# Kernel optimization log

Measured on AMD Instinct MI355X. Metric: run time of the kernel, lower is better.

Reference implementation:

```python
import jax, jax.numpy as jnp
import numpy as np

CUTOFF = 3.5          # angular_cutoff (init kwarg)
EPS = 1e-7            # keras.backend.epsilon()
CLIP_MIN = 1e-10      # tf.clip_by_value min on Carnot denominators
B, N = 8, 32
MLP_DIMS = [(9, 64), (64, 64), (64, 64), (64, 64), (64, 64), (64, 128), (128, 256)]


def _he(key, fan_in, fan_out):
    return jax.random.normal(key, (fan_in, fan_out), jnp.float32) * np.float32(np.sqrt(2.0 / fan_in))


def setup_inputs() -> dict:
    key = jax.random.key(0)
    k_pos, k_sp, k_w, k_b = jax.random.split(key, 4)
    # realistic symmetric distance matrix with zero diagonal, from random 3D positions
    pos = jax.random.uniform(k_pos, (B, N, 3), jnp.float32) * 9.0
    diff = pos[:, :, None, :] - pos[:, None, :, :]
    D = jnp.sqrt(jnp.sum(diff * diff, axis=-1) + 1e-12)
    D = D * (1.0 - jnp.eye(N, dtype=jnp.float32))
    species = jax.random.randint(k_sp, (B, N), 1, 10).astype(jnp.float32)
    inp = {"distance_matrices": D, "num_species_batch": species}
    for i, (fi, fo) in enumerate(MLP_DIMS):
        inp[f"W{i}"] = _he(jax.random.fold_in(k_w, i), fi, fo)
        inp[f"b{i}"] = jax.random.normal(jax.random.fold_in(k_b, i), (fo,), jnp.float32) * 0.01
    return inp


def _ang_mlp(x, W0, b0, W1, b1, W2, b2, W3, b3, W4, b4, W5, b5, W6, b6):
    # residual MLP: 9 -> 64 (x5, two residual adds) -> 128 -> 256, all tanh
    x_res = jnp.tanh(x @ W0 + b0)
    x1 = jnp.tanh(x_res @ W1 + b1)
    xb1 = x1 + x_res
    x2 = jnp.tanh(xb1 @ W2 + b2)
    x3 = jnp.tanh(x2 @ W3 + b3)
    x4 = jnp.tanh(x3 @ W4 + b4)
    xb2 = x4 + xb1
    xb3 = jnp.tanh(xb2 @ W5 + b5)
    return jnp.tanh(xb3 @ W6 + b6)


def _forward(D, S, W0, b0, W1, b1, W2, b2, W3, b3, W4, b4, W5, b5, W6, b6):
    n = D.shape[-1]
    ji, ki = jnp.triu_indices(n, k=1)                       # P = n(n-1)/2 ordered pairs j<k
    cm = (D < CUTOFF) & (D != 0.0)                          # [B,N,N]
    mask = cm[:, :, ji] & cm[:, :, ki]                      # [B,N,P] valid triplets (i;j,k)
    R_ij = D[:, :, ji]                                      # [B,N,P]
    R_ik = D[:, :, ki]
    R_jk = jnp.broadcast_to(D[:, ji, ki][:, None, :], R_ij.shape)
    z_i = jnp.broadcast_to(S[:, :, None], R_ij.shape)
    z_j = jnp.broadcast_to(S[:, ji][:, None, :], R_ij.shape)
    z_k = jnp.broadcast_to(S[:, ki][:, None, :], R_ij.shape)
    # Carnot formula for the three cosines of the triangle (i,j,k)
    clip = lambda d: jnp.maximum(d, CLIP_MIN)
    c_i = (R_ij**2 + R_ik**2 - R_jk**2) / clip(2.0 * R_ij * R_ik)
    c_j = (R_ij**2 + R_jk**2 - R_ik**2) / clip(2.0 * R_ij * R_jk)
    c_k = (R_ik**2 + R_jk**2 - R_ij**2) / clip(2.0 * R_ik * R_jk)
    geo = jnp.stack([
        R_ij + R_ik + R_jk,
        R_ij * R_ik + R_ij * R_jk + R_ik * R_jk,
        R_ij * R_ik * R_jk,
    ], axis=-1)                                             # [B,N,P,3]
    chem = jnp.stack([
        z_i + z_j + z_k,
        c_i + c_j + c_k,
        z_i * (z_j + z_k) + z_j * z_k - c_i * (c_j + c_k) - c_j * c_k,
        z_i * (c_j + c_k) + c_i * (z_j + z_k) + z_j * c_k + c_j * z_k,
        z_i * (z_j * z_k - c_j * c_k) - c_i * (z_j * c_k + c_j * z_k),
        z_i * (z_j * c_k + c_j * z_k) + c_i * (z_j * z_k - c_j * c_k),
    ], axis=-1)                                             # [B,N,P,6]
    geo = geo / (jnp.linalg.norm(geo, axis=-1, keepdims=True) + EPS)
    chem = chem / (jnp.linalg.norm(chem, axis=-1, keepdims=True) + EPS)
    feat = jnp.concatenate([geo, chem], axis=-1)            # [B,N,P,9]
    out = _ang_mlp(feat, W0, b0, W1, b1, W2, b2, W3, b3, W4, b4, W5, b5, W6, b6)  # [B,N,P,256]
    f_c = lambda d: 0.5 * jnp.cos(np.float32(np.pi) * d / CUTOFF) + 0.5
    w = jnp.where(mask, f_c(R_ij) * f_c(R_ik), 0.0)[..., None]
    GA = jnp.sum(out * w, axis=2)                           # scatter-add over triplets -> [B,N,256]
    return GA / (jnp.linalg.norm(GA, axis=-1, keepdims=True) + EPS)


def reference(distance_matrices, num_species_batch, W0, b0, W1, b1, W2, b2, W3, b3, W4, b4, W5, b5, W6, b6):
    return _forward(distance_matrices, num_species_batch, W0, b0, W1, b1, W2, b2, W3, b3, W4, b4, W5, b5, W6, b6)
```

## Files before the change

### kernel.cpp

```cpp
#include <hip/hip_runtime.h>
#include <math.h>

#define NB 8
#define NA 32
#define NCELL 256
#define NPAIR 496
#define SLOT 496
#define FST 10
#define TC 16
#define XS 20
#define NQ 8
#define CUTOFF_F 3.5f
#define EPS_F 1e-7f
#define CLIP_MIN_F 1e-10f
#define PI_F 3.14159274101257324f

__global__ __launch_bounds__(256) void aev_feat(
    const float* __restrict__ D, const float* __restrict__ S,
    float* __restrict__ feat, int* __restrict__ count, float* __restrict__ GA)
{
    __shared__ float Dm[NA][NA];
    __shared__ float Sv[NA];
    __shared__ int s_T;
    const int tid = threadIdx.x;
    const int cell = blockIdx.x;
    const int b = cell >> 5, i = cell & 31;

    for (int idx = tid; idx < NA * NA; idx += 256)
        ((float*)Dm)[idx] = D[b * NA * NA + idx];
    if (tid < NA) Sv[tid] = S[b * NA + tid];
    if (tid == 0) s_T = 0;
    GA[cell * 256 + tid] = 0.f;
    __syncthreads();

    for (int p = tid; p < NPAIR; p += 256) {
        int rem = p, j = 0;
        while (rem >= 31 - j) { rem -= 31 - j; ++j; }
        const int k = j + 1 + rem;
        const float dij = Dm[i][j], dik = Dm[i][k];
        if (dij < CUTOFF_F && dij != 0.f && dik < CUTOFF_F && dik != 0.f) {
            const int slot = atomicAdd(&s_T, 1);
            const float Rij = dij, Rik = dik, Rjk = Dm[j][k];
            const float zi = Sv[i], zj = Sv[j], zk = Sv[k];
            const float ci = (Rij*Rij + Rik*Rik - Rjk*Rjk) / fmaxf(2.f*Rij*Rik, CLIP_MIN_F);
            const float cj = (Rij*Rij + Rjk*Rjk - Rik*Rik) / fmaxf(2.f*Rij*Rjk, CLIP_MIN_F);
            const float ck = (Rik*Rik + Rjk*Rjk - Rij*Rij) / fmaxf(2.f*Rik*Rjk, CLIP_MIN_F);
            float g0 = Rij + Rik + Rjk;
            float g1 = Rij*Rik + Rij*Rjk + Rik*Rjk;
            float g2 = Rij*Rik*Rjk;
            const float gn = sqrtf(g0*g0 + g1*g1 + g2*g2) + EPS_F;
            float h0 = zi + zj + zk;
            float h1 = ci + cj + ck;
            float h2 = zi*(zj + zk) + zj*zk - ci*(cj + ck) - cj*ck;
            float h3 = zi*(cj + ck) + ci*(zj + zk) + zj*ck + cj*zk;
            float h4 = zi*(zj*zk - cj*ck) - ci*(zj*ck + cj*zk);
            float h5 = zi*(zj*ck + cj*zk) + ci*(zj*zk - cj*ck);
            const float hn = sqrtf(h0*h0 + h1*h1 + h2*h2 + h3*h3 + h4*h4 + h5*h5) + EPS_F;
            const float fcij = 0.5f * cosf(PI_F * Rij / CUTOFF_F) + 0.5f;
            const float fcik = 0.5f * cosf(PI_F * Rik / CUTOFF_F) + 0.5f;
            float* fp = &feat[(cell * SLOT + slot) * FST];
            fp[0] = g0 / gn; fp[1] = g1 / gn; fp[2] = g2 / gn;
            fp[3] = h0 / hn; fp[4] = h1 / hn; fp[5] = h2 / hn;
            fp[6] = h3 / hn; fp[7] = h4 / hn; fp[8] = h5 / hn;
            fp[9] = fcij * fcik;
        }
    }
    __syncthreads();
    if (tid == 0) count[cell] = s_T;
}

__device__ __forceinline__ void cp_async16(const float* g, float* l) {
    __builtin_amdgcn_global_load_lds(
        (const __attribute__((address_space(1))) unsigned int*)g,
        (__attribute__((address_space(3))) unsigned int*)l, 16, 0, 0);
}

__device__ __forceinline__ void stage16k(const float* __restrict__ g,
                                         float* __restrict__ buf, int tid) {
    const int lane = tid & 63, w = tid >> 6;
#pragma unroll
    for (int r = 0; r < 4; ++r) {
        const int off = (w * 4 + r) * 256;
        cp_async16(g + off + lane * 4, buf + off);
    }
}

template<int K, bool RES>
__device__ __forceinline__ void compute64(
    const float* __restrict__ Wl, const float* __restrict__ bl,
    const float* __restrict__ X, float* __restrict__ Y,
    const float* __restrict__ R, int tid)
{
    const int fi = tid & 63;
    const int xo = (tid >> 6) * 4;
    const float bb = bl[fi];
    float a0 = bb, a1 = bb, a2 = bb, a3 = bb;
#pragma unroll 4
    for (int k = 0; k < K; ++k) {
        const float4 xv = *(const float4*)&X[k * XS + xo];
        const float w = Wl[k * 64 + fi];
        a0 += xv.x * w; a1 += xv.y * w; a2 += xv.z * w; a3 += xv.w * w;
    }
    float4 y;
    y.x = tanhf(a0); y.y = tanhf(a1); y.z = tanhf(a2); y.w = tanhf(a3);
    if (RES) {
        const float4 r = *(const float4*)&R[fi * XS + xo];
        y.x += r.x; y.y += r.y; y.z += r.z; y.w += r.w;
    }
    *(float4*)&Y[fi * XS + xo] = y;
}

__device__ __forceinline__ void compute5_part(
    const float* __restrict__ Wl , const float* __restrict__ X,
    int k0, float (&a0)[4], float (&a1)[4], int tid)
{
    const int fo = tid & 63;
    const int xo = (tid >> 6) * 4;
#pragma unroll 4
    for (int k = 0; k < 32; ++k) {
        const float4 xv = *(const float4*)&X[(k0 + k) * XS + xo];
        const float w0 = Wl[k * 128 + fo];
        const float w1 = Wl[k * 128 + fo + 64];
        a0[0] += xv.x * w0; a0[1] += xv.y * w0; a0[2] += xv.z * w0; a0[3] += xv.w * w0;
        a1[0] += xv.x * w1; a1[1] += xv.y * w1; a1[2] += xv.z * w1; a1[3] += xv.w * w1;
    }
}

__device__ __forceinline__ void compute6_part(
    const float* __restrict__ Wl , const float* __restrict__ X,
    int k0, float (&a)[16], int tid)
{
#pragma unroll 2
    for (int k = 0; k < 16; ++k) {
        const float w = Wl[k * 256 + tid];
        const float4 x0 = *(const float4*)&X[(k0 + k) * XS + 0];
        const float4 x1 = *(const float4*)&X[(k0 + k) * XS + 4];
        const float4 x2 = *(const float4*)&X[(k0 + k) * XS + 8];
        const float4 x3 = *(const float4*)&X[(k0 + k) * XS + 12];
        a[0]  += x0.x * w; a[1]  += x0.y * w; a[2]  += x0.z * w; a[3]  += x0.w * w;
        a[4]  += x1.x * w; a[5]  += x1.y * w; a[6]  += x1.z * w; a[7]  += x1.w * w;
        a[8]  += x2.x * w; a[9]  += x2.y * w; a[10] += x2.z * w; a[11] += x2.w * w;
        a[12] += x3.x * w; a[13] += x3.y * w; a[14] += x3.z * w; a[15] += x3.w * w;
    }
}

__global__ __launch_bounds__(256, 2) void aev_mlp(
    const float* __restrict__ feat, const int* __restrict__ count,
    const float* __restrict__ W0, const float* __restrict__ b0,
    const float* __restrict__ W1, const float* __restrict__ b1,
    const float* __restrict__ W2, const float* __restrict__ b2,
    const float* __restrict__ W3, const float* __restrict__ b3,
    const float* __restrict__ W4, const float* __restrict__ b4,
    const float* __restrict__ W5, const float* __restrict__ b5,
    const float* __restrict__ W6, const float* __restrict__ b6,
    float* __restrict__ GA)
{
    __shared__ __align__(16) float WB0[4096];
    __shared__ __align__(16) float WB1[4096];
    __shared__ __align__(16) float WB2[4096];
    __shared__ __align__(16) float Xs[9 * XS];
    __shared__ __align__(16) float U0[64 * XS];
    __shared__ __align__(16) float U1[64 * XS];
    __shared__ __align__(16) float U2[64 * XS];
    __shared__ __align__(16) float U3[128 * XS];
    __shared__ float wsh[TC];
    __shared__ float bsh[704];

    const int tid = threadIdx.x;
    const int cell = blockIdx.x & 255;
    const int q = blockIdx.x >> 8;
    const int T = count[cell];
    const int nch = (T + TC - 1) / TC;
    if (q >= nch) return;

    if (tid < 64) {
        bsh[tid]       = b0[tid];
        bsh[64 + tid]  = b1[tid];
        bsh[128 + tid] = b2[tid];
        bsh[192 + tid] = b3[tid];
        bsh[256 + tid] = b4[tid];
    }
    if (tid < 128) bsh[320 + tid] = b5[tid];
    bsh[448 + tid] = b6[tid];

    float gacc = 0.f;

    for (int c = q; c < nch; c += NQ) {
        const int t0 = c * TC;

        stage16k(W1, WB1, tid);
        if (tid < 144) ((float4*)WB0)[tid] = ((const float4*)W0)[tid];
        if (tid < TC * FST) {
            const int t = tid / FST, qf = tid % FST;
            const int slot = t0 + t;
            const float v = (slot < T) ? feat[(cell * SLOT + t0) * FST + tid] : 0.f;
            if (qf == 9) wsh[t] = v; else Xs[qf * XS + t] = v;
        }
        __syncthreads();

        stage16k(W2, WB2, tid);
        compute64<9,  false>(WB0, bsh + 0,   Xs, U0, nullptr, tid);
        __syncthreads();
        stage16k(W3, WB0, tid);
        compute64<64, true >(WB1, bsh + 64,  U0, U1, U0, tid);
        __syncthreads();
        stage16k(W4, WB1, tid);
        compute64<64, false>(WB2, bsh + 128, U1, U2, nullptr, tid);
        __syncthreads();
        stage16k(W5, WB2, tid);
        compute64<64, false>(WB0, bsh + 192, U2, U0, nullptr, tid);
        __syncthreads();
        stage16k(W5 + 4096, WB0, tid);
        compute64<64, true >(WB1, bsh + 256, U0, U2, U1, tid);
        __syncthreads();

        float a0[4], a1[4];
        {
            const int fo = tid & 63;
            const float bb0 = bsh[320 + fo], bb1 = bsh[320 + fo + 64];
#pragma unroll
            for (int r = 0; r < 4; ++r) { a0[r] = bb0; a1[r] = bb1; }
        }
        stage16k(W6, WB1, tid);
        compute5_part(WB2, U2, 0, a0, a1, tid);
        __syncthreads();
        stage16k(W6 + 4096, WB2, tid);
        compute5_part(WB0, U2, 32, a0, a1, tid);
        {
            const int fo = tid & 63;
            const int xo = (tid >> 6) * 4;
            float4 y0, y1;
            y0.x = tanhf(a0[0]); y0.y = tanhf(a0[1]); y0.z = tanhf(a0[2]); y0.w = tanhf(a0[3]);
            y1.x = tanhf(a1[0]); y1.y = tanhf(a1[1]); y1.z = tanhf(a1[2]); y1.w = tanhf(a1[3]);
            *(float4*)&U3[fo * XS + xo] = y0;
            *(float4*)&U3[(fo + 64) * XS + xo] = y1;
        }
        __syncthreads();

        float a6[16];
        {
            const float bb = bsh[448 + tid];
#pragma unroll
            for (int r = 0; r < 16; ++r) a6[r] = bb;
        }
        stage16k(W6 + 2 * 4096, WB0, tid);
        compute6_part(WB1, U3, 0, a6, tid);
        __syncthreads();
        stage16k(W6 + 3 * 4096, WB1, tid);
        compute6_part(WB2, U3, 16, a6, tid);
        __syncthreads();
        stage16k(W6 + 4 * 4096, WB2, tid);
        compute6_part(WB0, U3, 32, a6, tid);
        __syncthreads();
        stage16k(W6 + 5 * 4096, WB0, tid);
        compute6_part(WB1, U3, 48, a6, tid);
        __syncthreads();
        stage16k(W6 + 6 * 4096, WB1, tid);
        compute6_part(WB2, U3, 64, a6, tid);
        __syncthreads();
        stage16k(W6 + 7 * 4096, WB2, tid);
        compute6_part(WB0, U3, 80, a6, tid);
        __syncthreads();
        compute6_part(WB1, U3, 96, a6, tid);
        __syncthreads();
        compute6_part(WB2, U3, 112, a6, tid);

#pragma unroll 4
        for (int r = 0; r < 16; ++r)
            gacc += wsh[r] * tanhf(a6[r]);
        __syncthreads();
    }

    atomicAdd(&GA[cell * 256 + tid], gacc);
}

__global__ __launch_bounds__(256) void aev_norm(
    const float* __restrict__ GA, float* __restrict__ out)
{
    __shared__ float wred[4];
    const int tid = threadIdx.x;
    const int cell = blockIdx.x;
    const float v = GA[cell * 256 + tid];
    float ss = v * v;
#pragma unroll
    for (int off = 32; off > 0; off >>= 1) ss += __shfl_down(ss, off);
    if ((tid & 63) == 0) wred[tid >> 6] = ss;
    __syncthreads();
    const float tot = wred[0] + wred[1] + wred[2] + wred[3];
    out[cell * 256 + tid] = v / (sqrtf(tot) + EPS_F);
}

extern "C" void kernel_launch(void* const* d_in, const int* in_sizes, int n_in,
                              void* d_out, int out_size, void* d_ws, size_t ws_size,
                              hipStream_t stream)
{
    const float* D  = (const float*)d_in[0];
    const float* S  = (const float*)d_in[1];
    const float* W0 = (const float*)d_in[2];  const float* b0 = (const float*)d_in[3];
    const float* W1 = (const float*)d_in[4];  const float* b1 = (const float*)d_in[5];
    const float* W2 = (const float*)d_in[6];  const float* b2 = (const float*)d_in[7];
    const float* W3 = (const float*)d_in[8];  const float* b3 = (const float*)d_in[9];
    const float* W4 = (const float*)d_in[10]; const float* b4 = (const float*)d_in[11];
    const float* W5 = (const float*)d_in[12]; const float* b5 = (const float*)d_in[13];
    const float* W6 = (const float*)d_in[14]; const float* b6 = (const float*)d_in[15];
    float* out = (float*)d_out;

    float* feat  = (float*)d_ws;
    int*   count = (int*)(feat + NCELL * SLOT * FST);
    float* GA    = (float*)(count + 256);

    aev_feat<<<dim3(NCELL), dim3(256), 0, stream>>>(D, S, feat, count, GA);
    aev_mlp<<<dim3(NCELL * NQ), dim3(256), 0, stream>>>(
        feat, count, W0, b0, W1, b1, W2, b2, W3, b3, W4, b4, W5, b5, W6, b6, GA);
    aev_norm<<<dim3(NCELL), dim3(256), 0, stream>>>(GA, out);
}
```

Baseline: 117.9 us.

## Double triplet chunk size and retile MLP layers for larger per-thread register tiles

Raises the per-chunk triplet tile from 16 to 32, so each staged weight block in shared memory is reused across twice as many triplets. Per-thread register tiles grow to 8 columns in the 64-wide layers and to 2×16 outputs in the 256-wide layer. The grid is reorganised to four blocks per cell instead of eight, and the launch bound asking for two blocks per SM is dropped. This cuts weight staging and synchronisation per triplet, but raises register pressure and lowers block count and occupancy.

```diff
diff --git a/kernel.cpp b/kernel.cpp
--- a/kernel.cpp
+++ b/kernel.cpp
@@ -7,9 +7,9 @@
 #define NPAIR 496
 #define SLOT 496
 #define FST 10
-#define TC 16
-#define XS 20
-#define NQ 8
+#define TC 32
+#define XS 36
+#define NQ 4
 #define CUTOFF_F 3.5f
 #define EPS_F 1e-7f
 #define CLIP_MIN_F 1e-10f
@@ -92,59 +92,74 @@
     const float* __restrict__ R, int tid)
 {
     const int fi = tid & 63;
-    const int xo = (tid >> 6) * 4;
+    const int xo = (tid >> 6) * 8;
     const float bb = bl[fi];
-    float a0 = bb, a1 = bb, a2 = bb, a3 = bb;
+    float a[8];
+#pragma unroll
+    for (int r = 0; r < 8; ++r) a[r] = bb;
 #pragma unroll 4
     for (int k = 0; k < K; ++k) {
-        const float4 xv = *(const float4*)&X[k * XS + xo];
+        const float4 x0 = *(const float4*)&X[k * XS + xo];
+        const float4 x1 = *(const float4*)&X[k * XS + xo + 4];
         const float w = Wl[k * 64 + fi];
-        a0 += xv.x * w; a1 += xv.y * w; a2 += xv.z * w; a3 += xv.w * w;
-    }
-    float4 y;
-    y.x = tanhf(a0); y.y = tanhf(a1); y.z = tanhf(a2); y.w = tanhf(a3);
+        a[0] += x0.x * w; a[1] += x0.y * w; a[2] += x0.z * w; a[3] += x0.w * w;
+        a[4] += x1.x * w; a[5] += x1.y * w; a[6] += x1.z * w; a[7] += x1.w * w;
+    }
+    float4 y0, y1;
+    y0.x = tanhf(a[0]); y0.y = tanhf(a[1]); y0.z = tanhf(a[2]); y0.w = tanhf(a[3]);
+    y1.x = tanhf(a[4]); y1.y = tanhf(a[5]); y1.z = tanhf(a[6]); y1.w = tanhf(a[7]);
     if (RES) {
-        const float4 r = *(const float4*)&R[fi * XS + xo];
-        y.x += r.x; y.y += r.y; y.z += r.z; y.w += r.w;
-    }
-    *(float4*)&Y[fi * XS + xo] = y;
+        const float4 r0 = *(const float4*)&R[fi * XS + xo];
+        const float4 r1 = *(const float4*)&R[fi * XS + xo + 4];
+        y0.x += r0.x; y0.y += r0.y; y0.z += r0.z; y0.w += r0.w;
+        y1.x += r1.x; y1.y += r1.y; y1.z += r1.z; y1.w += r1.w;
+    }
+    *(float4*)&Y[fi * XS + xo]     = y0;
+    *(float4*)&Y[fi * XS + xo + 4] = y1;
 }
 
 __device__ __forceinline__ void compute5_part(
     const float* __restrict__ Wl , const float* __restrict__ X,
-    int k0, float (&a0)[4], float (&a1)[4], int tid)
+    int k0, float (&a0)[8], float (&a1)[8], int tid)
 {
     const int fo = tid & 63;
-    const int xo = (tid >> 6) * 4;
-#pragma unroll 4
+    const int xo = (tid >> 6) * 8;
+#pragma unroll 2
     for (int k = 0; k < 32; ++k) {
-        const float4 xv = *(const float4*)&X[(k0 + k) * XS + xo];
+        const float4 x0 = *(const float4*)&X[(k0 + k) * XS + xo];
+        const float4 x1 = *(const float4*)&X[(k0 + k) * XS + xo + 4];
         const float w0 = Wl[k * 128 + fo];
         const float w1 = Wl[k * 128 + fo + 64];
-        a0[0] += xv.x * w0; a0[1] += xv.y * w0; a0[2] += xv.z * w0; a0[3] += xv.w * w0;
-        a1[0] += xv.x * w1; a1[1] += xv.y * w1; a1[2] += xv.z * w1; a1[3] += xv.w * w1;
+        a0[0] += x0.x * w0; a0[1] += x0.y * w0; a0[2] += x0.z * w0; a0[3] += x0.w * w0;
+        a0[4] += x1.x * w0; a0[5] += x1.y * w0; a0[6] += x1.z * w0; a0[7] += x1.w * w0;
+        a1[0] += x0.x * w1; a1[1] += x0.y * w1; a1[2] += x0.z * w1; a1[3] += x0.w * w1;
+        a1[4] += x1.x * w1; a1[5] += x1.y * w1; a1[6] += x1.z * w1; a1[7] += x1.w * w1;
     }
 }
 
 __device__ __forceinline__ void compute6_part(
     const float* __restrict__ Wl , const float* __restrict__ X,
-    int k0, float (&a)[16], int tid)
+    int fo, int to, float (&a0)[16], float (&a1)[16])
 {
 #pragma unroll 2
     for (int k = 0; k < 16; ++k) {
-        const float w = Wl[k * 256 + tid];
-        const float4 x0 = *(const float4*)&X[(k0 + k) * XS + 0];
-        const float4 x1 = *(const float4*)&X[(k0 + k) * XS + 4];
-        const float4 x2 = *(const float4*)&X[(k0 + k) * XS + 8];
-        const float4 x3 = *(const float4*)&X[(k0 + k) * XS + 12];
-        a[0]  += x0.x * w; a[1]  += x0.y * w; a[2]  += x0.z * w; a[3]  += x0.w * w;
-        a[4]  += x1.x * w; a[5]  += x1.y * w; a[6]  += x1.z * w; a[7]  += x1.w * w;
-        a[8]  += x2.x * w; a[9]  += x2.y * w; a[10] += x2.z * w; a[11] += x2.w * w;
-        a[12] += x3.x * w; a[13] += x3.y * w; a[14] += x3.z * w; a[15] += x3.w * w;
-    }
-}
-
-__global__ __launch_bounds__(256, 2) void aev_mlp(
+        const float2 wv = *(const float2*)&Wl[k * 256 + fo];
+        const float4 x0 = *(const float4*)&X[k * XS + to];
+        const float4 x1 = *(const float4*)&X[k * XS + to + 4];
+        const float4 x2 = *(const float4*)&X[k * XS + to + 8];
+        const float4 x3 = *(const float4*)&X[k * XS + to + 12];
+        a0[0]  += x0.x * wv.x; a0[1]  += x0.y * wv.x; a0[2]  += x0.z * wv.x; a0[3]  += x0.w * wv.x;
+        a0[4]  += x1.x * wv.x; a0[5]  += x1.y * wv.x; a0[6]  += x1.z * wv.x; a0[7]  += x1.w * wv.x;
+        a0[8]  += x2.x * wv.x; a0[9]  += x2.y * wv.x; a0[10] += x2.z * wv.x; a0[11] += x2.w * wv.x;
+        a0[12] += x3.x * wv.x; a0[13] += x3.y * wv.x; a0[14] += x3.z * wv.x; a0[15] += x3.w * wv.x;
+        a1[0]  += x0.x * wv.y; a1[1]  += x0.y * wv.y; a1[2]  += x0.z * wv.y; a1[3]  += x0.w * wv.y;
+        a1[4]  += x1.x * wv.y; a1[5]  += x1.y * wv.y; a1[6]  += x1.z * wv.y; a1[7]  += x1.w * wv.y;
+        a1[8]  += x2.x * wv.y; a1[9]  += x2.y * wv.y; a1[10] += x2.z * wv.y; a1[11] += x2.w * wv.y;
+        a1[12] += x3.x * wv.y; a1[13] += x3.y * wv.y; a1[14] += x3.z * wv.y; a1[15] += x3.w * wv.y;
+    }
+}
+
+__global__ __launch_bounds__(256) void aev_mlp(
     const float* __restrict__ feat, const int* __restrict__ count,
     const float* __restrict__ W0, const float* __restrict__ b0,
     const float* __restrict__ W1, const float* __restrict__ b1,
@@ -167,8 +182,8 @@
     __shared__ float bsh[704];
 
     const int tid = threadIdx.x;
-    const int cell = blockIdx.x & 255;
-    const int q = blockIdx.x >> 8;
+    const int cell = blockIdx.x >> 2;
+    const int q = blockIdx.x & 3;
     const int T = count[cell];
     const int nch = (T + TC - 1) / TC;
     if (q >= nch) return;
@@ -183,17 +198,19 @@
     if (tid < 128) bsh[320 + tid] = b5[tid];
     bsh[448 + tid] = b6[tid];
 
-    float gacc = 0.f;
+    const int fo6 = (tid & 127) * 2;
+    const int to6 = (tid >> 7) * 16;
+    float gacc0 = 0.f, gacc1 = 0.f;
 
     for (int c = q; c < nch; c += NQ) {
         const int t0 = c * TC;
 
         stage16k(W1, WB1, tid);
         if (tid < 144) ((float4*)WB0)[tid] = ((const float4*)W0)[tid];
-        if (tid < TC * FST) {
-            const int t = tid / FST, qf = tid % FST;
+        for (int idx = tid; idx < TC * FST; idx += 256) {
+            const int t = idx / FST, qf = idx % FST;
             const int slot = t0 + t;
-            const float v = (slot < T) ? feat[(cell * SLOT + t0) * FST + tid] : 0.f;
+            const float v = (slot < T) ? feat[(cell * SLOT + t0) * FST + idx] : 0.f;
             if (qf == 9) wsh[t] = v; else Xs[qf * XS + t] = v;
         }
         __syncthreads();
@@ -214,12 +231,12 @@
         compute64<64, true >(WB1, bsh + 256, U0, U2, U1, tid);
         __syncthreads();
 
-        float a0[4], a1[4];
+        float a0[8], a1[8];
         {
             const int fo = tid & 63;
             const float bb0 = bsh[320 + fo], bb1 = bsh[320 + fo + 64];
 #pragma unroll
-            for (int r = 0; r < 4; ++r) { a0[r] = bb0; a1[r] = bb1; }
+            for (int r = 0; r < 8; ++r) { a0[r] = bb0; a1[r] = bb1; }
         }
         stage16k(W6, WB1, tid);
         compute5_part(WB2, U2, 0, a0, a1, tid);
@@ -228,50 +245,60 @@
         compute5_part(WB0, U2, 32, a0, a1, tid);
         {
             const int fo = tid & 63;
-            const int xo = (tid >> 6) * 4;
+            const int xo = (tid >> 6) * 8;
             float4 y0, y1;
             y0.x = tanhf(a0[0]); y0.y = tanhf(a0[1]); y0.z = tanhf(a0[2]); y0.w = tanhf(a0[3]);
-            y1.x = tanhf(a1[0]); y1.y = tanhf(a1[1]); y1.z = tanhf(a1[2]); y1.w = tanhf(a1[3]);
-            *(float4*)&U3[fo * XS + xo] = y0;
-            *(float4*)&U3[(fo + 64) * XS + xo] = y1;
-        }
-        __syncthreads();
-
-        float a6[16];
+            y1.x = tanhf(a0[4]); y1.y = tanhf(a0[5]); y1.z = tanhf(a0[6]); y1.w = tanhf(a0[7]);
+            *(float4*)&U3[fo * XS + xo]     = y0;
+            *(float4*)&U3[fo * XS + xo + 4] = y1;
+            y0.x = tanhf(a1[0]); y0.y = tanhf(a1[1]); y0.z = tanhf(a1[2]); y0.w = tanhf(a1[3]);
+            y1.x = tanhf(a1[4]); y1.y = tanhf(a1[5]); y1.z = tanhf(a1[6]); y1.w = tanhf(a1[7]);
+            *(float4*)&U3[(fo + 64) * XS + xo]     = y0;
+            *(float4*)&U3[(fo + 64) * XS + xo + 4] = y1;
+        }
+        __syncthreads();
+
+        float c0[16], c1[16];
         {
-            const float bb = bsh[448 + tid];
-#pragma unroll
-            for (int r = 0; r < 16; ++r) a6[r] = bb;
+            const float bb0 = bsh[448 + fo6], bb1 = bsh[448 + fo6 + 1];
+#pragma unroll
+            for (int r = 0; r < 16; ++r) { c0[r] = bb0; c1[r] = bb1; }
         }
         stage16k(W6 + 2 * 4096, WB0, tid);
-        compute6_part(WB1, U3, 0, a6, tid);
+        compute6_part(WB1, U3 + 0 * XS * 16 + 0, fo6, to6, c0, c1);
         __syncthreads();
         stage16k(W6 + 3 * 4096, WB1, tid);
-        compute6_part(WB2, U3, 16, a6, tid);
+        compute6_part(WB2, U3 + 16 * XS, fo6, to6, c0, c1);
         __syncthreads();
         stage16k(W6 + 4 * 4096, WB2, tid);
-        compute6_part(WB0, U3, 32, a6, tid);
+        compute6_part(WB0, U3 + 32 * XS, fo6, to6, c0, c1);
         __syncthreads();
         stage16k(W6 + 5 * 4096, WB0, tid);
-        compute6_part(WB1, U3, 48, a6, tid);
+        compute6_part(WB1, U3 + 48 * XS, fo6, to6, c0, c1);
         __syncthreads();
         stage16k(W6 + 6 * 4096, WB1, tid);
-        compute6_part(WB2, U3, 64, a6, tid);
+        compute6_part(WB2, U3 + 64 * XS, fo6, to6, c0, c1);
         __syncthreads();
         stage16k(W6 + 7 * 4096, WB2, tid);
-        compute6_part(WB0, U3, 80, a6, tid);
-        __syncthreads();
-        compute6_part(WB1, U3, 96, a6, tid);
-        __syncthreads();
-        compute6_part(WB2, U3, 112, a6, tid);
-
+        compute6_part(WB0, U3 + 80 * XS, fo6, to6, c0, c1);
+        __syncthreads();
+        compute6_part(WB1, U3 + 96 * XS, fo6, to6, c0, c1);
+        __syncthreads();
+        compute6_part(WB2, U3 + 112 * XS, fo6, to6, c0, c1);
+
+        float s0 = 0.f, s1 = 0.f;
 #pragma unroll 4
-        for (int r = 0; r < 16; ++r)
-            gacc += wsh[r] * tanhf(a6[r]);
-        __syncthreads();
-    }
-
-    atomicAdd(&GA[cell * 256 + tid], gacc);
+        for (int r = 0; r < 16; ++r) {
+            const float wt = wsh[to6 + r];
+            s0 += wt * tanhf(c0[r]);
+            s1 += wt * tanhf(c1[r]);
+        }
+        gacc0 += s0; gacc1 += s1;
+        __syncthreads();
+    }
+
+    atomicAdd(&GA[cell * 256 + fo6], gacc0);
+    atomicAdd(&GA[cell * 256 + fo6 + 1], gacc1);
 }
 
 __global__ __launch_bounds__(256) void aev_norm(
```

New measurement: 223.8 us. 89.9% more time.

## Shrink MLP shared memory to double-buffered weights and register biases

Applied to the files above, without the earlier changes.

Replaces the triple-buffered weight staging with two 16 KB buffers plus a small persistent W0 copy, and reuses U0/U1 in place of the separate U3 buffer. Biases now live in registers instead of a shared array. The launch-bounds minimum-blocks hint is dropped. The intent is to cut LDS use so more blocks fit per CU, at the cost of a shallower prefetch pipeline (one stage ahead instead of two) and extra register pressure.

```diff
diff --git a/kernel.cpp b/kernel.cpp
--- a/kernel.cpp
+++ b/kernel.cpp
@@ -87,13 +87,12 @@
 
 template<int K, bool RES>
 __device__ __forceinline__ void compute64(
-    const float* __restrict__ Wl, const float* __restrict__ bl,
+    const float* __restrict__ Wl, float bb,
     const float* __restrict__ X, float* __restrict__ Y,
     const float* __restrict__ R, int tid)
 {
     const int fi = tid & 63;
     const int xo = (tid >> 6) * 4;
-    const float bb = bl[fi];
     float a0 = bb, a1 = bb, a2 = bb, a3 = bb;
 #pragma unroll 4
     for (int k = 0; k < K; ++k) {
@@ -128,15 +127,15 @@
 
 __device__ __forceinline__ void compute6_part(
     const float* __restrict__ Wl , const float* __restrict__ X,
-    int k0, float (&a)[16], int tid)
+    float (&a)[16], int tid)
 {
 #pragma unroll 2
     for (int k = 0; k < 16; ++k) {
         const float w = Wl[k * 256 + tid];
-        const float4 x0 = *(const float4*)&X[(k0 + k) * XS + 0];
-        const float4 x1 = *(const float4*)&X[(k0 + k) * XS + 4];
-        const float4 x2 = *(const float4*)&X[(k0 + k) * XS + 8];
-        const float4 x3 = *(const float4*)&X[(k0 + k) * XS + 12];
+        const float4 x0 = *(const float4*)&X[k * XS + 0];
+        const float4 x1 = *(const float4*)&X[k * XS + 4];
+        const float4 x2 = *(const float4*)&X[k * XS + 8];
+        const float4 x3 = *(const float4*)&X[k * XS + 12];
         a[0]  += x0.x * w; a[1]  += x0.y * w; a[2]  += x0.z * w; a[3]  += x0.w * w;
         a[4]  += x1.x * w; a[5]  += x1.y * w; a[6]  += x1.z * w; a[7]  += x1.w * w;
         a[8]  += x2.x * w; a[9]  += x2.y * w; a[10] += x2.z * w; a[11] += x2.w * w;
@@ -144,7 +143,7 @@
     }
 }
 
-__global__ __launch_bounds__(256, 2) void aev_mlp(
+__global__ __launch_bounds__(256) void aev_mlp(
     const float* __restrict__ feat, const int* __restrict__ count,
     const float* __restrict__ W0, const float* __restrict__ b0,
     const float* __restrict__ W1, const float* __restrict__ b1,
@@ -155,16 +154,14 @@
     const float* __restrict__ W6, const float* __restrict__ b6,
     float* __restrict__ GA)
 {
-    __shared__ __align__(16) float WB0[4096];
-    __shared__ __align__(16) float WB1[4096];
-    __shared__ __align__(16) float WB2[4096];
+    __shared__ __align__(16) float WA[4096];
+    __shared__ __align__(16) float WBf[4096];
+    __shared__ __align__(16) float W0s[576];
     __shared__ __align__(16) float Xs[9 * XS];
     __shared__ __align__(16) float U0[64 * XS];
     __shared__ __align__(16) float U1[64 * XS];
     __shared__ __align__(16) float U2[64 * XS];
-    __shared__ __align__(16) float U3[128 * XS];
     __shared__ float wsh[TC];
-    __shared__ float bsh[704];
 
     const int tid = threadIdx.x;
     const int cell = blockIdx.x & 255;
@@ -173,23 +170,23 @@
     const int nch = (T + TC - 1) / TC;
     if (q >= nch) return;
 
-    if (tid < 64) {
-        bsh[tid]       = b0[tid];
-        bsh[64 + tid]  = b1[tid];
-        bsh[128 + tid] = b2[tid];
-        bsh[192 + tid] = b3[tid];
-        bsh[256 + tid] = b4[tid];
-    }
-    if (tid < 128) bsh[320 + tid] = b5[tid];
-    bsh[448 + tid] = b6[tid];
+    const int fi64 = tid & 63;
+    const float bias0 = b0[fi64];
+    const float bias1 = b1[fi64];
+    const float bias2 = b2[fi64];
+    const float bias3 = b3[fi64];
+    const float bias4 = b4[fi64];
+    const float bias5a = b5[fi64];
+    const float bias5b = b5[fi64 + 64];
+    const float bias6 = b6[tid];
+
+    if (tid < 144) ((float4*)W0s)[tid] = ((const float4*)W0)[tid];
 
     float gacc = 0.f;
 
     for (int c = q; c < nch; c += NQ) {
         const int t0 = c * TC;
 
-        stage16k(W1, WB1, tid);
-        if (tid < 144) ((float4*)WB0)[tid] = ((const float4*)W0)[tid];
         if (tid < TC * FST) {
             const int t = tid / FST, qf = tid % FST;
             const int slot = t0 + t;
@@ -198,72 +195,66 @@
         }
         __syncthreads();
 
-        stage16k(W2, WB2, tid);
-        compute64<9,  false>(WB0, bsh + 0,   Xs, U0, nullptr, tid);
-        __syncthreads();
-        stage16k(W3, WB0, tid);
-        compute64<64, true >(WB1, bsh + 64,  U0, U1, U0, tid);
-        __syncthreads();
-        stage16k(W4, WB1, tid);
-        compute64<64, false>(WB2, bsh + 128, U1, U2, nullptr, tid);
-        __syncthreads();
-        stage16k(W5, WB2, tid);
-        compute64<64, false>(WB0, bsh + 192, U2, U0, nullptr, tid);
-        __syncthreads();
-        stage16k(W5 + 4096, WB0, tid);
-        compute64<64, true >(WB1, bsh + 256, U0, U2, U1, tid);
+        stage16k(W1, WA, tid);
+        compute64<9,  false>(W0s, bias0, Xs, U0, nullptr, tid);
+        __syncthreads();
+        stage16k(W2, WBf, tid);
+        compute64<64, true >(WA, bias1, U0, U1, U0, tid);
+        __syncthreads();
+        stage16k(W3, WA, tid);
+        compute64<64, false>(WBf, bias2, U1, U2, nullptr, tid);
+        __syncthreads();
+        stage16k(W4, WBf, tid);
+        compute64<64, false>(WA, bias3, U2, U0, nullptr, tid);
+        __syncthreads();
+        stage16k(W5, WA, tid);
+        compute64<64, true >(WBf, bias4, U0, U2, U1, tid);
         __syncthreads();
 
         float a0[4], a1[4];
-        {
-            const int fo = tid & 63;
-            const float bb0 = bsh[320 + fo], bb1 = bsh[320 + fo + 64];
 #pragma unroll
-            for (int r = 0; r < 4; ++r) { a0[r] = bb0; a1[r] = bb1; }
-        }
-        stage16k(W6, WB1, tid);
-        compute5_part(WB2, U2, 0, a0, a1, tid);
-        __syncthreads();
-        stage16k(W6 + 4096, WB2, tid);
-        compute5_part(WB0, U2, 32, a0, a1, tid);
+        for (int r = 0; r < 4; ++r) { a0[r] = bias5a; a1[r] = bias5b; }
+        stage16k(W5 + 4096, WBf, tid);
+        compute5_part(WA, U2, 0, a0, a1, tid);
+        __syncthreads();
+        stage16k(W6, WA, tid);
+        compute5_part(WBf, U2, 32, a0, a1, tid);
         {
             const int fo = tid & 63;
             const int xo = (tid >> 6) * 4;
             float4 y0, y1;
             y0.x = tanhf(a0[0]); y0.y = tanhf(a0[1]); y0.z = tanhf(a0[2]); y0.w = tanhf(a0[3]);
             y1.x = tanhf(a1[0]); y1.y = tanhf(a1[1]); y1.z = tanhf(a1[2]); y1.w = tanhf(a1[3]);
-            *(float4*)&U3[fo * XS + xo] = y0;
-            *(float4*)&U3[(fo + 64) * XS + xo] = y1;
+            *(float4*)&U0[fo * XS + xo] = y0;
+            *(float4*)&U1[fo * XS + xo] = y1;
         }
         __syncthreads();
 
         float a6[16];
-        {
-            const float bb = bsh[448 + tid];
 #pragma unroll
-            for (int r = 0; r < 16; ++r) a6[r] = bb;
-        }
-        stage16k(W6 + 2 * 4096, WB0, tid);
-        compute6_part(WB1, U3, 0, a6, tid);
-        __syncthreads();
-        stage16k(W6 + 3 * 4096, WB1, tid);
-        compute6_part(WB2, U3, 16, a6, tid);
-        __syncthreads();
-        stage16k(W6 + 4 * 4096, WB2, tid);
-        compute6_part(WB0, U3, 32, a6, tid);
-        __syncthreads();
-        stage16k(W6 + 5 * 4096, WB0, tid);
-        compute6_part(WB1, U3, 48, a6, tid);
-        __syncthreads();
-        stage16k(W6 + 6 * 4096, WB1, tid);
-        compute6_part(WB2, U3, 64, a6, tid);
-        __syncthreads();
-        stage16k(W6 + 7 * 4096, WB2, tid);
-        compute6_part(WB0, U3, 80, a6, tid);
-        __syncthreads();
-        compute6_part(WB1, U3, 96, a6, tid);
-        __syncthreads();
-        compute6_part(WB2, U3, 112, a6, tid);
+        for (int r = 0; r < 16; ++r) a6[r] = bias6;
+        stage16k(W6 + 1 * 4096, WBf, tid);
+        compute6_part(WA, U0 + 0 * XS, a6, tid);
+        __syncthreads();
+        stage16k(W6 + 2 * 4096, WA, tid);
+        compute6_part(WBf, U0 + 16 * XS, a6, tid);
+        __syncthreads();
+        stage16k(W6 + 3 * 4096, WBf, tid);
+        compute6_part(WA, U0 + 32 * XS, a6, tid);
+        __syncthreads();
+        stage16k(W6 + 4 * 4096, WA, tid);
+        compute6_part(WBf, U0 + 48 * XS, a6, tid);
+        __syncthreads();
+        stage16k(W6 + 5 * 4096, WBf, tid);
+        compute6_part(WA, U1 + 0 * XS, a6, tid);
+        __syncthreads();
+        stage16k(W6 + 6 * 4096, WA, tid);
+        compute6_part(WBf, U1 + 16 * XS, a6, tid);
+        __syncthreads();
+        stage16k(W6 + 7 * 4096, WBf, tid);
+        compute6_part(WA, U1 + 32 * XS, a6, tid);
+        __syncthreads();
+        compute6_part(WBf, U1 + 48 * XS, a6, tid);
 
 #pragma unroll 4
         for (int r = 0; r < 16; ++r)
```

Result: slower. 120.5 us (+2.2%).
